# Kernel optimization log

Hardware: AMD Instinct MI355X
Metric: run time of the kernel (lower is better)

Reference implementation:

```python
import jax, jax.numpy as jnp
import numpy as np

DIM = 256
HEADS = 8
DIM_HEAD = 64
INNER = HEADS * DIM_HEAD  # 512
B, N = 4, 1024


def setup_inputs() -> dict:
    key = jax.random.key(0)
    ks = jax.random.split(key, 7)
    x = jax.random.normal(ks[0], (B, N, DIM), dtype=jnp.float32)
    attn_bias = jax.random.normal(ks[1], (B, HEADS, N, N), dtype=jnp.float32)
    s = 1.0 / np.sqrt(DIM)
    Wq = jax.random.normal(ks[2], (DIM, INNER), dtype=jnp.float32) * s
    Wkv = jax.random.normal(ks[3], (DIM, 2 * INNER), dtype=jnp.float32) * s
    # to_out initialized to zero in the torch module; use small random so output is non-trivial
    Wo = jax.random.normal(ks[4], (INNER, DIM), dtype=jnp.float32) * (1.0 / np.sqrt(INNER))
    bo = jnp.zeros((DIM,), dtype=jnp.float32)
    # gating initialized weight=0, bias=1 -> sigmoid(1); use small random weight + bias 1
    Wg = jax.random.normal(ks[5], (DIM, INNER), dtype=jnp.float32) * 0.02
    bg = jnp.ones((INNER,), dtype=jnp.float32)
    return {"x": x, "attn_bias": attn_bias, "Wq": Wq, "Wkv": Wkv,
            "Wo": Wo, "bo": bo, "Wg": Wg, "bg": bg}


def reference(x, attn_bias, Wq, Wkv, Wo, bo, Wg, bg):
    b, n, _ = x.shape
    scale = DIM_HEAD ** -0.5
    q = x @ Wq                                    # [b, n, inner]
    kv = x @ Wkv                                  # [b, n, 2*inner]
    k, v = jnp.split(kv, 2, axis=-1)
    def split_heads(t):
        return t.reshape(b, n, HEADS, DIM_HEAD).transpose(0, 2, 1, 3)  # [b,h,n,d]
    q, k, v = split_heads(q) * scale, split_heads(k), split_heads(v)
    dots = jnp.einsum('bhid,bhjd->bhij', q, k) + attn_bias
    # explicit max-subtract then softmax (matches original; numerically identical)
    attn = jax.nn.softmax(dots, axis=-1)
    out = jnp.einsum('bhij,bhjd->bhid', attn, v)  # [b,h,n,d]
    out = out.transpose(0, 2, 1, 3).reshape(b, n, INNER)
    gates = jax.nn.sigmoid(x @ Wg + bg)
    out = out * gates
    return out @ Wo + bo
```

## Files before the change

### kernel.cpp

```cpp
#include <hip/hip_runtime.h>

typedef unsigned short u16;
typedef unsigned int u32;
typedef __attribute__((ext_vector_type(8))) __bf16 bf16x8;
typedef __attribute__((ext_vector_type(4))) float floatx4;
typedef const __attribute__((address_space(1))) unsigned char glob_u8;
typedef __attribute__((address_space(3))) unsigned char lds_u8;

#define DEV __device__ __forceinline__

DEV u16 f2bf(float f) {
  return __builtin_bit_cast(u16, (__bf16)f);
}
DEV float bf2f(u16 h) {
  u32 u = ((u32)h) << 16;
  return __builtin_bit_cast(float, u);
}
DEV floatx4 MFMA(bf16x8 a, bf16x8 b, floatx4 c) {
  return __builtin_amdgcn_mfma_f32_16x16x32_bf16(a, b, c, 0, 0, 0);
}

__global__ void convert_k(const float* __restrict__ x, const float* __restrict__ Wq,
                          const float* __restrict__ Wkv, const float* __restrict__ Wg,
                          const float* __restrict__ Wo,
                          u16* __restrict__ xb, u16* __restrict__ WcatT, u16* __restrict__ WoT) {
  int i = blockIdx.x * 256 + threadIdx.x;
  if (i < 1048576) { xb[i] = f2bf(x[i]); return; }
  i -= 1048576;
  if (i < 524288) {
    int n = i >> 8, kk = i & 255;
    float v;
    if (n < 512) v = Wq[kk * 512 + n];
    else if (n < 1536) v = Wkv[kk * 1024 + (n - 512)];
    else v = Wg[kk * 512 + (n - 1536)];
    WcatT[i] = f2bf(v);
    return;
  }
  i -= 524288;
  if (i < 131072) {
    int n = i >> 9, kk = i & 511;
    WoT[i] = f2bf(Wo[kk * 256 + n]);
  }
}

__global__ __launch_bounds__(256, 4) void gemm_qkvg(
    const u16* __restrict__ xb, const u16* __restrict__ WcatT, const float* __restrict__ bg,
    u16* __restrict__ qb, u16* __restrict__ kfrag, u16* __restrict__ vfrag, u16* __restrict__ gb) {
  __shared__ __attribute__((aligned(16))) u16 As[128 * 40];
  __shared__ __attribute__((aligned(16))) u16 Bs[64 * 40];
  const int tid = threadIdx.x;
  const int wave = tid >> 6, lane = tid & 63;
  const int lane15 = lane & 15, quad = lane >> 4;
  const int rm0 = blockIdx.x * 128;
  const int cn0 = blockIdx.y * 64;
  const int wm = (wave & 1) * 64, wn = (wave >> 1) * 32;
  const int rowA = tid >> 1, segA = (tid & 1) * 16;
  const int rowB = tid >> 2, segB = (tid & 3) * 8;
  floatx4 acc[4][2] = {};
  uint4 a0 = *(const uint4*)(xb + (rm0 + rowA) * 256 + segA);
  uint4 a1 = *(const uint4*)(xb + (rm0 + rowA) * 256 + segA + 8);
  uint4 b0 = *(const uint4*)(WcatT + (cn0 + rowB) * 256 + segB);
#pragma unroll 1
  for (int k0 = 0; k0 < 256; k0 += 32) {
    __syncthreads();
    *(uint4*)(As + rowA * 40 + segA) = a0;
    *(uint4*)(As + rowA * 40 + segA + 8) = a1;
    *(uint4*)(Bs + rowB * 40 + segB) = b0;
    __syncthreads();
    if (k0 < 224) {
      a0 = *(const uint4*)(xb + (rm0 + rowA) * 256 + k0 + 32 + segA);
      a1 = *(const uint4*)(xb + (rm0 + rowA) * 256 + k0 + 32 + segA + 8);
      b0 = *(const uint4*)(WcatT + (cn0 + rowB) * 256 + k0 + 32 + segB);
    }
    bf16x8 af[4], bfr[2];
#pragma unroll
    for (int mt = 0; mt < 4; ++mt) af[mt] = *(const bf16x8*)(As + (wm + mt * 16 + lane15) * 40 + quad * 8);
#pragma unroll
    for (int nt = 0; nt < 2; ++nt) bfr[nt] = *(const bf16x8*)(Bs + (wn + nt * 16 + lane15) * 40 + quad * 8);
#pragma unroll
    for (int mt = 0; mt < 4; ++mt)
#pragma unroll
      for (int nt = 0; nt < 2; ++nt)
        acc[mt][nt] = MFMA(af[mt], bfr[nt], acc[mt][nt]);
  }
#pragma unroll
  for (int mt = 0; mt < 4; ++mt)
#pragma unroll
    for (int nt = 0; nt < 2; ++nt)
#pragma unroll
      for (int r = 0; r < 4; ++r) {
        int row = rm0 + wm + mt * 16 + quad * 4 + r;
        int col = cn0 + wn + nt * 16 + lane15;
        float v = acc[mt][nt][r];
        int b = row >> 10, n = row & 1023;
        if (col < 512) {
          int h = col >> 6, d = col & 63;
          qb[((b * 8 + h) * 1024 + n) * 64 + d] = f2bf(v * 0.125f);
        } else if (col < 1024) {
          int c = col - 512, h = c >> 6, d = c & 63;
          int bh2 = b * 8 + h;
          int t = n >> 4, l15 = n & 15;
          int half = d >> 5, qd = (d >> 3) & 3, e = d & 7;
          kfrag[(size_t)bh2 * 65536 + t * 1024 + half * 512 + (qd * 16 + l15) * 8 + e] = f2bf(v);
        } else if (col < 1536) {
          int c = col - 1024, h = c >> 6, d = c & 63;
          int bh2 = b * 8 + h;
          int t64 = n >> 6, ck = (n >> 5) & 1, qd = (n >> 3) & 3, e = n & 7;
          int dt = d >> 4, l15 = d & 15;
          vfrag[(size_t)bh2 * 65536 + t64 * 4096 + dt * 1024 + ck * 512 + (qd * 16 + l15) * 8 + e] = f2bf(v);
        } else {
          int c = col - 1536;
          float g = 1.0f / (1.0f + __expf(-(v + bg[c])));
          gb[row * 512 + c] = f2bf(g);
        }
      }
}

__global__ __launch_bounds__(256, 4) void attn_k(
    const u16* __restrict__ qb, const u16* __restrict__ kfrag, const u16* __restrict__ vfrag,
    const float* __restrict__ bias, const u16* __restrict__ gb, u16* __restrict__ ogb) {
  __shared__ __attribute__((aligned(16))) u16 Kt[2][4096];
  __shared__ __attribute__((aligned(16))) u16 Vt[2][4096];
  __shared__ __attribute__((aligned(16))) u16 Ps[4 * 16 * 40];
  const int tid = threadIdx.x;
  const int wave = tid >> 6, lane = tid & 63;
  const int lane15 = lane & 15, quad = lane >> 4;
  const int bh = blockIdx.x;
  const int q0 = blockIdx.y * 32;
  const int qw = (wave & 1) * 16;
  const int kh = wave >> 1;

  bf16x8 qf0, qf1;
  {
    const u16* qrow = qb + ((size_t)(bh * 1024 + q0 + qw + lane15)) * 64 + quad * 8;
    qf0 = *(const bf16x8*)(qrow);
    qf1 = *(const bf16x8*)(qrow + 32);
  }
  bf16x8 ones;
#pragma unroll
  for (int e = 0; e < 8; ++e) ones[e] = __builtin_bit_cast(__bf16, (u16)0x3F80);

  floatx4 oacc[4] = {};
  floatx4 lacc = {};

  u16* Pw = Ps + wave * (16 * 40);
  const u16* kp = kfrag + (size_t)bh * 65536;
  const u16* vp = vfrag + (size_t)bh * 65536;
  const float* bbase = bias + ((size_t)(bh * 1024 + q0 + qw + quad * 4)) * 1024 + kh * 32 + lane15;

  auto stage = [&](int kt, int bufi) {
    const u16* kS = kp + kt * 4096;
    const u16* vS = vp + kt * 4096;
#pragma unroll
    for (int c = 0; c < 2; ++c) {
      int ch = wave * 2 + c;
      __builtin_amdgcn_global_load_lds((glob_u8*)(kS + ch * 512 + lane * 8),
                                       (lds_u8*)(&Kt[bufi][ch * 512]), 16, 0, 0);
      __builtin_amdgcn_global_load_lds((glob_u8*)(vS + ch * 512 + lane * 8),
                                       (lds_u8*)(&Vt[bufi][ch * 512]), 16, 0, 0);
    }
  };

  stage(0, 0);
  __syncthreads();
  int cur = 0;
#pragma unroll 1
  for (int kt = 0; kt < 16; ++kt) {
    if (kt < 15) stage(kt + 1, cur ^ 1);
    float bv[4][2];
#pragma unroll
    for (int r = 0; r < 4; ++r)
#pragma unroll
      for (int j = 0; j < 2; ++j)
        bv[r][j] = bbase[r * 1024 + kt * 64 + j * 16];
    const u16* Ktc = Kt[cur];
    const u16* Vtc = Vt[cur];
    floatx4 s[2];
#pragma unroll
    for (int j = 0; j < 2; ++j) {
      const u16* kb = Ktc + (kh * 2 + j) * 1024 + lane * 8;
      bf16x8 kf0 = *(const bf16x8*)(kb);
      bf16x8 kf1 = *(const bf16x8*)(kb + 512);
      floatx4 z = {};
      z = MFMA(qf0, kf0, z);
      s[j] = MFMA(qf1, kf1, z);
    }
#pragma unroll
    for (int j = 0; j < 2; ++j)
#pragma unroll
      for (int r = 0; r < 4; ++r)
        s[j][r] = __expf(s[j][r] + bv[r][j] - 8.0f);
#pragma unroll
    for (int j = 0; j < 2; ++j)
#pragma unroll
      for (int r = 0; r < 4; ++r)
        Pw[(quad * 4 + r) * 40 + j * 16 + lane15] = f2bf(s[j][r]);
    bf16x8 pf = *(const bf16x8*)(Pw + lane15 * 40 + quad * 8);

    lacc = MFMA(pf, ones, lacc);
#pragma unroll
    for (int dt = 0; dt < 4; ++dt) {
      bf16x8 vf = *(const bf16x8*)(Vtc + dt * 1024 + kh * 512 + lane * 8);
      oacc[dt] = MFMA(pf, vf, oacc[dt]);
    }
    __syncthreads();
    cur ^= 1;
  }

  float* red = (float*)Kt;
  if (wave >= 2) {
    float* r0 = red + (wave - 2) * 1280 + lane * 20;
#pragma unroll
    for (int dt = 0; dt < 4; ++dt)
#pragma unroll
      for (int r = 0; r < 4; ++r) r0[dt * 4 + r] = oacc[dt][r];
#pragma unroll
    for (int r = 0; r < 4; ++r) r0[16 + r] = lacc[r];
  }
  __syncthreads();
  if (wave < 2) {
    const float* r0 = red + wave * 1280 + lane * 20;
#pragma unroll
    for (int dt = 0; dt < 4; ++dt)
#pragma unroll
      for (int r = 0; r < 4; ++r) oacc[dt][r] += r0[dt * 4 + r];
#pragma unroll
    for (int r = 0; r < 4; ++r) lacc[r] += r0[16 + r];

    const int b = bh >> 3, h = bh & 7;
#pragma unroll
    for (int r = 0; r < 4; ++r) {
      int q = q0 + wave * 16 + quad * 4 + r;
      float inv = 1.0f / lacc[r];
      size_t base = ((size_t)(b * 1024 + q)) * 512 + h * 64;
#pragma unroll
      for (int dt = 0; dt < 4; ++dt) {
        size_t gi = base + dt * 16 + lane15;
        ogb[gi] = f2bf(oacc[dt][r] * inv * bf2f(gb[gi]));
      }
    }
  }
}

__global__ __launch_bounds__(256, 4) void gemm_out_k(
    const u16* __restrict__ og, const u16* __restrict__ WoT,
    const float* __restrict__ bo, float* __restrict__ out) {
  __shared__ __attribute__((aligned(16))) u16 As[64 * 40];
  __shared__ __attribute__((aligned(16))) u16 Bs[64 * 40];
  const int tid = threadIdx.x;
  const int wave = tid >> 6, lane = tid & 63;
  const int lane15 = lane & 15, quad = lane >> 4;
  const int rm0 = blockIdx.x * 64;
  const int cn0 = blockIdx.y * 64;
  const int wm = (wave & 1) * 32, wn = (wave >> 1) * 32;
  const int rowA = tid >> 2, segA = (tid & 3) * 8;
  floatx4 acc[2][2] = {};
  uint4 a0 = *(const uint4*)(og + (rm0 + rowA) * 512 + segA);
  uint4 b0 = *(const uint4*)(WoT + (cn0 + rowA) * 512 + segA);
#pragma unroll 1
  for (int k0 = 0; k0 < 512; k0 += 32) {
    __syncthreads();
    *(uint4*)(As + rowA * 40 + segA) = a0;
    *(uint4*)(Bs + rowA * 40 + segA) = b0;
    __syncthreads();
    if (k0 < 480) {
      a0 = *(const uint4*)(og + (rm0 + rowA) * 512 + k0 + 32 + segA);
      b0 = *(const uint4*)(WoT + (cn0 + rowA) * 512 + k0 + 32 + segA);
    }
    bf16x8 af[2], bfr[2];
#pragma unroll
    for (int mt = 0; mt < 2; ++mt) af[mt] = *(const bf16x8*)(As + (wm + mt * 16 + lane15) * 40 + quad * 8);
#pragma unroll
    for (int nt = 0; nt < 2; ++nt) bfr[nt] = *(const bf16x8*)(Bs + (wn + nt * 16 + lane15) * 40 + quad * 8);
#pragma unroll
    for (int mt = 0; mt < 2; ++mt)
#pragma unroll
      for (int nt = 0; nt < 2; ++nt)
        acc[mt][nt] = MFMA(af[mt], bfr[nt], acc[mt][nt]);
  }
#pragma unroll
  for (int nt = 0; nt < 2; ++nt) {
    int col = cn0 + wn + nt * 16 + lane15;
    float bv = bo[col];
#pragma unroll
    for (int mt = 0; mt < 2; ++mt)
#pragma unroll
      for (int r = 0; r < 4; ++r) {
        int row = rm0 + wm + mt * 16 + quad * 4 + r;
        out[(size_t)row * 256 + col] = acc[mt][nt][r] + bv;
      }
  }
}

extern "C" void kernel_launch(void* const* d_in, const int* in_sizes, int n_in,
                              void* d_out, int out_size, void* d_ws, size_t ws_size,
                              hipStream_t stream) {
  const float* x = (const float*)d_in[0];
  const float* bias = (const float*)d_in[1];
  const float* Wq = (const float*)d_in[2];
  const float* Wkv = (const float*)d_in[3];
  const float* Wo = (const float*)d_in[4];
  const float* bo = (const float*)d_in[5];
  const float* Wg = (const float*)d_in[6];
  const float* bg = (const float*)d_in[7];
  float* out = (float*)d_out;
  char* ws = (char*)d_ws;
  u16* xb    = (u16*)(ws);
  u16* WcatT = (u16*)(ws + 2097152);
  u16* WoT   = (u16*)(ws + 3145728);
  u16* qb    = (u16*)(ws + 3407872);
  u16* kfrag = (u16*)(ws + 7602176);
  u16* vfrag = (u16*)(ws + 11796480);
  u16* gb    = (u16*)(ws + 15990784);
  u16* ogb   = (u16*)(ws + 20185088);

  convert_k<<<6656, 256, 0, stream>>>(x, Wq, Wkv, Wg, Wo, xb, WcatT, WoT);
  dim3 g1(32, 32);
  gemm_qkvg<<<g1, 256, 0, stream>>>(xb, WcatT, bg, qb, kfrag, vfrag, gb);
  dim3 g2(32, 32);
  attn_k<<<g2, 256, 0, stream>>>(qb, kfrag, vfrag, bias, gb, ogb);
  dim3 g3(64, 4);
  gemm_out_k<<<g3, 256, 0, stream>>>(ogb, WoT, bo, out);
}
```

Baseline: 253.3 us.

## Pre-tile GEMM operands into MFMA fragment layout and stage via global_load_lds

The conversion kernel now writes x and the concatenated QKV/gate weights in a tiled, MFMA-fragment-ordered bf16 layout, vectorizing the x conversion to 8 elements per thread. The projection GEMM then loads each k-tile directly from global memory into double-buffered LDS with global_load_lds and reads fragments contiguously, removing the register round-trip and one barrier per iteration. This cuts conversion launch size and GEMM staging overhead. It relies on the async LDS loads completing before the single barrier, which is an implicit synchronisation assumption.

```diff
diff --git a/kernel.cpp b/kernel.cpp
--- a/kernel.cpp
+++ b/kernel.cpp
@@ -23,20 +23,42 @@
 __global__ void convert_k(const float* __restrict__ x, const float* __restrict__ Wq,
                           const float* __restrict__ Wkv, const float* __restrict__ Wg,
                           const float* __restrict__ Wo,
-                          u16* __restrict__ xb, u16* __restrict__ WcatT, u16* __restrict__ WoT) {
+                          u16* __restrict__ xA, u16* __restrict__ WB, u16* __restrict__ WoT) {
   int i = blockIdx.x * 256 + threadIdx.x;
-  if (i < 1048576) { xb[i] = f2bf(x[i]); return; }
-  i -= 1048576;
-  if (i < 524288) {
-    int n = i >> 8, kk = i & 255;
-    float v;
-    if (n < 512) v = Wq[kk * 512 + n];
-    else if (n < 1536) v = Wkv[kk * 1024 + (n - 512)];
-    else v = Wg[kk * 512 + (n - 1536)];
-    WcatT[i] = f2bf(v);
+  if (i < 131072) {
+    int tile = i >> 9, w = i & 511;
+    int g = w >> 6, q = (w >> 4) & 3, l15 = w & 15;
+    int rb = tile >> 3, kb = tile & 7;
+    int row = rb * 128 + g * 16 + l15;
+    int k0 = kb * 32 + q * 8;
+    float4 v0 = *(const float4*)(x + row * 256 + k0);
+    float4 v1 = *(const float4*)(x + row * 256 + k0 + 4);
+    u16 o[8] = {f2bf(v0.x), f2bf(v0.y), f2bf(v0.z), f2bf(v0.w),
+                f2bf(v1.x), f2bf(v1.y), f2bf(v1.z), f2bf(v1.w)};
+    *(uint4*)(xA + (size_t)i * 8) = *(uint4*)o;
     return;
   }
-  i -= 524288;
+  i -= 131072;
+  if (i < 65536) {
+    int tile = i >> 8, w = i & 255;
+    int g = (w >> 6) & 3, q = (w >> 4) & 3, l15 = w & 15;
+    int nb = tile >> 3, kb = tile & 7;
+    int n = nb * 64 + g * 16 + l15;
+    int k0 = kb * 32 + q * 8;
+    u16 o[8];
+#pragma unroll
+    for (int e = 0; e < 8; ++e) {
+      int k = k0 + e;
+      float v;
+      if (n < 512) v = Wq[k * 512 + n];
+      else if (n < 1536) v = Wkv[k * 1024 + (n - 512)];
+      else v = Wg[k * 512 + (n - 1536)];
+      o[e] = f2bf(v);
+    }
+    *(uint4*)(WB + (size_t)i * 8) = *(uint4*)o;
+    return;
+  }
+  i -= 65536;
   if (i < 131072) {
     int n = i >> 9, kk = i & 511;
     WoT[i] = f2bf(Wo[kk * 256 + n]);
@@ -44,44 +66,56 @@
 }
 
 __global__ __launch_bounds__(256, 4) void gemm_qkvg(
-    const u16* __restrict__ xb, const u16* __restrict__ WcatT, const float* __restrict__ bg,
+    const u16* __restrict__ xA, const u16* __restrict__ WB, const float* __restrict__ bg,
     u16* __restrict__ qb, u16* __restrict__ kfrag, u16* __restrict__ vfrag, u16* __restrict__ gb) {
-  __shared__ __attribute__((aligned(16))) u16 As[128 * 40];
-  __shared__ __attribute__((aligned(16))) u16 Bs[64 * 40];
+  __shared__ __attribute__((aligned(16))) u16 As[2][4096];
+  __shared__ __attribute__((aligned(16))) u16 Bs[2][2048];
   const int tid = threadIdx.x;
   const int wave = tid >> 6, lane = tid & 63;
   const int lane15 = lane & 15, quad = lane >> 4;
-  const int rm0 = blockIdx.x * 128;
-  const int cn0 = blockIdx.y * 64;
+  const int rb = blockIdx.x;
+  const int nb = blockIdx.y;
+  const int rm0 = rb * 128;
+  const int cn0 = nb * 64;
   const int wm = (wave & 1) * 64, wn = (wave >> 1) * 32;
-  const int rowA = tid >> 1, segA = (tid & 1) * 16;
-  const int rowB = tid >> 2, segB = (tid & 3) * 8;
+  const int ga = (wave & 1) * 4;
+  const int gb2 = (wave >> 1) * 2;
+
   floatx4 acc[4][2] = {};
-  uint4 a0 = *(const uint4*)(xb + (rm0 + rowA) * 256 + segA);
-  uint4 a1 = *(const uint4*)(xb + (rm0 + rowA) * 256 + segA + 8);
-  uint4 b0 = *(const uint4*)(WcatT + (cn0 + rowB) * 256 + segB);
+
+  auto stage = [&](int kb, int bufi) {
+    const u16* At = xA + ((size_t)(rb * 8 + kb)) * 4096;
+    const u16* Bt = WB + ((size_t)(nb * 8 + kb)) * 2048;
+#pragma unroll
+    for (int c = 0; c < 2; ++c) {
+      int ch = wave * 2 + c;
+      __builtin_amdgcn_global_load_lds((glob_u8*)(At + ch * 512 + lane * 8),
+                                       (lds_u8*)(&As[bufi][ch * 512]), 16, 0, 0);
+    }
+    __builtin_amdgcn_global_load_lds((glob_u8*)(Bt + wave * 512 + lane * 8),
+                                     (lds_u8*)(&Bs[bufi][wave * 512]), 16, 0, 0);
+  };
+
+  stage(0, 0);
+  __syncthreads();
+  int cur = 0;
 #pragma unroll 1
-  for (int k0 = 0; k0 < 256; k0 += 32) {
-    __syncthreads();
-    *(uint4*)(As + rowA * 40 + segA) = a0;
-    *(uint4*)(As + rowA * 40 + segA + 8) = a1;
-    *(uint4*)(Bs + rowB * 40 + segB) = b0;
-    __syncthreads();
-    if (k0 < 224) {
-      a0 = *(const uint4*)(xb + (rm0 + rowA) * 256 + k0 + 32 + segA);
-      a1 = *(const uint4*)(xb + (rm0 + rowA) * 256 + k0 + 32 + segA + 8);
-      b0 = *(const uint4*)(WcatT + (cn0 + rowB) * 256 + k0 + 32 + segB);
-    }
+  for (int kb = 0; kb < 8; ++kb) {
+    if (kb < 7) stage(kb + 1, cur ^ 1);
+    const u16* Ac = As[cur];
+    const u16* Bc = Bs[cur];
     bf16x8 af[4], bfr[2];
 #pragma unroll
-    for (int mt = 0; mt < 4; ++mt) af[mt] = *(const bf16x8*)(As + (wm + mt * 16 + lane15) * 40 + quad * 8);
-#pragma unroll
-    for (int nt = 0; nt < 2; ++nt) bfr[nt] = *(const bf16x8*)(Bs + (wn + nt * 16 + lane15) * 40 + quad * 8);
+    for (int mt = 0; mt < 4; ++mt) af[mt] = *(const bf16x8*)(Ac + ((ga + mt) * 64 + lane) * 8);
+#pragma unroll
+    for (int nt = 0; nt < 2; ++nt) bfr[nt] = *(const bf16x8*)(Bc + ((gb2 + nt) * 64 + lane) * 8);
 #pragma unroll
     for (int mt = 0; mt < 4; ++mt)
 #pragma unroll
       for (int nt = 0; nt < 2; ++nt)
         acc[mt][nt] = MFMA(af[mt], bfr[nt], acc[mt][nt]);
+    __syncthreads();
+    cur ^= 1;
   }
 #pragma unroll
   for (int mt = 0; mt < 4; ++mt)
@@ -305,8 +339,8 @@
   const float* bg = (const float*)d_in[7];
   float* out = (float*)d_out;
   char* ws = (char*)d_ws;
-  u16* xb    = (u16*)(ws);
-  u16* WcatT = (u16*)(ws + 2097152);
+  u16* xA    = (u16*)(ws);
+  u16* WB    = (u16*)(ws + 2097152);
   u16* WoT   = (u16*)(ws + 3145728);
   u16* qb    = (u16*)(ws + 3407872);
   u16* kfrag = (u16*)(ws + 7602176);
@@ -314,9 +348,9 @@
   u16* gb    = (u16*)(ws + 15990784);
   u16* ogb   = (u16*)(ws + 20185088);
 
-  convert_k<<<6656, 256, 0, stream>>>(x, Wq, Wkv, Wg, Wo, xb, WcatT, WoT);
+  convert_k<<<1280, 256, 0, stream>>>(x, Wq, Wkv, Wg, Wo, xA, WB, WoT);
   dim3 g1(32, 32);
-  gemm_qkvg<<<g1, 256, 0, stream>>>(xb, WcatT, bg, qb, kfrag, vfrag, gb);
+  gemm_qkvg<<<g1, 256, 0, stream>>>(xA, WB, bg, qb, kfrag, vfrag, gb);
   dim3 g2(32, 32);
   attn_k<<<g2, 256, 0, stream>>>(qb, kfrag, vfrag, bias, gb, ogb);
   dim3 g3(64, 4);
```

Result: faster. 248.0 us (-2.1%).
